# Optimization experiments

Hardware: AMD Instinct MI355X
Metric: run time of the kernel (lower is better)

## Reference

```python
import jax, jax.numpy as jnp
import numpy as np

HEAD_DIM = 128
SCALE = HEAD_DIM ** -0.5  # head_scaling == up_scaling == 1/sqrt(head_dim)


def setup_inputs() -> dict:
    key = jax.random.key(0)
    kq, kk, ku, kv = jax.random.split(key, 4)
    B, H, S, D = 2, 16, 2048, 128
    Hk, I = 4, 2048
    Q = jax.random.normal(kq, (B, H, S, D), dtype=jnp.float32)
    K = jax.random.normal(kk, (Hk, I, D), dtype=jnp.float32)
    U = jax.random.normal(ku, (Hk, I, D), dtype=jnp.float32)
    V = jax.random.normal(kv, (Hk, I, D), dtype=jnp.float32)
    return {"Q": Q, "K": K, "U": U, "V": V}


def reference(Q, K, U, V):
    # Q: (B, H, S, D); K/U/V: (Hk, I, D); GQA grouping G = H // Hk
    B, H, S, D = Q.shape
    Hk, I, _ = K.shape
    G = H // Hk
    Qr = Q.reshape(B, Hk, G, S, D)
    # gate scores and up projection, both scaled by 1/sqrt(D)
    M = jnp.einsum('bkgsd,kid->bkgsi', Qr, K) * SCALE
    N = jnp.einsum('bkgsd,kid->bkgsi', Qr, U) * SCALE
    A = jax.nn.silu(M) * N  # gated activation, (B, Hk, G, S, I)
    out = jnp.einsum('bkgsi,kid->bkgsd', A, V)
    return out.reshape(B, H, S, D)
```

## Files before the change

### kernel.cpp

```cpp
#include <hip/hip_runtime.h>

#define B_   2
#define H_   16
#define G_   4
#define S_   2048
#define D_   128
#define I_   2048

#define BM   128
#define BN   32
#define TPB  256
#define NIT  (I_ / BN)
#define KUT  4096
#define VT   8192
#define HSTR (3 * 262144)

#define KIDX(r,c) ((r)*128 + ((c) ^ (((r)&15)<<3)))
#define VIDX(d,c) ((d)*64  + ((c) ^ (((d)&7)<<3)))

static constexpr float SCALE = 0.08838834764831845f;

typedef __fp16   p2v  __attribute__((ext_vector_type(2)));
typedef _Float16 h8v  __attribute__((ext_vector_type(8)));
typedef float    f4v  __attribute__((ext_vector_type(4)));
typedef float    f16v __attribute__((ext_vector_type(16)));
typedef int      i4v  __attribute__((ext_vector_type(4)));

__device__ __forceinline__ int pkf16(float a, float b) {
    p2v t = __builtin_amdgcn_cvt_pkrtz(a, b);
    int r; __builtin_memcpy(&r, &t, 4); return r;
}

#define GL_LDS(gp, lp) __builtin_amdgcn_global_load_lds(                      \
    (const __attribute__((address_space(1))) void*)(gp),                      \
    (__attribute__((address_space(3))) void*)(lp), 16, 0, 0)

__global__ __launch_bounds__(256) void convert_kernel(
    const float* __restrict__ Kg, const float* __restrict__ Ug,
    const float* __restrict__ Vg, _Float16* __restrict__ ws)
{
    const int bid = blockIdx.x;
    const int tid = threadIdx.x;
    __shared__ float vt[64 * 128];
    if (bid < 256) {
        const int kh = bid >> 6, m = (bid >> 5) & 1, it = bid & 31;
        const float* src = (m ? Ug : Kg) + (size_t)kh * I_ * D_ + (size_t)it * 64 * D_;
        _Float16* dstb = ws + (size_t)kh * HSTR + (size_t)m * 262144 + (size_t)it * 2 * KUT;
        const int r   = tid >> 2;
        const int cb  = (tid & 3) * 32;
        const int swz = (r & 15) << 3;
        _Float16* dst = dstb + (size_t)(r >> 5) * KUT + (r & 31) * 128;
#pragma unroll
        for (int g = 0; g < 4; ++g) {
            const int cc0 = cb + g * 8;
            const int d0  = cc0 ^ swz;
            const float4 a = *(const float4*)(src + r * D_ + d0);
            const float4 c = *(const float4*)(src + r * D_ + d0 + 4);
            h8v v; p2v* v2 = (p2v*)&v;
            v2[0] = __builtin_amdgcn_cvt_pkrtz(a.x, a.y);
            v2[1] = __builtin_amdgcn_cvt_pkrtz(a.z, a.w);
            v2[2] = __builtin_amdgcn_cvt_pkrtz(c.x, c.y);
            v2[3] = __builtin_amdgcn_cvt_pkrtz(c.z, c.w);
            *(h8v*)(dst + cc0) = v;
        }
    } else {
        const int v  = bid - 256;
        const int kh = v >> 5, it = v & 31;
        const float* src = Vg + (size_t)kh * I_ * D_ + (size_t)it * 64 * D_;
#pragma unroll
        for (int p = 0; p < 8; ++p) {
            const int idx = p * 256 + tid;
            const int i   = idx >> 5;
            const int d4  = (idx & 31) * 4;
            *(float4*)(&vt[i * 128 + d4]) = *(const float4*)(src + (size_t)i * D_ + d4);
        }
        __syncthreads();
        _Float16* dst = ws + (size_t)kh * HSTR + 2 * 262144 + (size_t)it * VT;
        const int d   = tid >> 1;
        const int cb  = (tid & 1) * 32;
        const int swz = (d & 7) << 3;
#pragma unroll
        for (int g = 0; g < 4; ++g) {
            const int cc0 = cb + g * 8;
            const int ib  = cc0 ^ swz;
            h8v w; p2v* w2 = (p2v*)&w;
#pragma unroll
            for (int pr = 0; pr < 4; ++pr)
                w2[pr] = __builtin_amdgcn_cvt_pkrtz(vt[(ib + 2 * pr) * 128 + d],
                                                    vt[(ib + 2 * pr + 1) * 128 + d]);
            *(h8v*)(dst + d * 64 + cc0) = w;
        }
    }
}

__global__ __launch_bounds__(TPB, 2) void flashmlp_kernel(
    const float* __restrict__ Qg, const _Float16* __restrict__ ws,
    float* __restrict__ Og)
{
    __shared__ _Float16 Ks[2 * KUT];
    __shared__ _Float16 Us[2 * KUT];
    __shared__ _Float16 Vt[2 * VT];

    const int bid   = blockIdx.x;
    const int xcd   = bid & 7;
    const int kh    = xcd >> 1;
    const int j     = ((bid >> 3) << 1) | (xcd & 1);
    const int stile = j & 15;
    const int bg    = j >> 4;
    const int b     = bg >> 2;
    const int g     = bg & 3;
    const int h     = kh * G_ + g;

    const int tid  = threadIdx.x;
    const int wave = tid >> 6;
    const int lane = tid & 63;
    const int l31  = lane & 31;
    const int hl   = lane >> 5;

    const size_t qbase = ((size_t)(b * H_ + h) * S_ + (size_t)stile * BM) * D_;
    const _Float16* wsK = ws + (size_t)kh * HSTR;
    const _Float16* wsU = wsK + 262144;
    const _Float16* wsV = wsK + 2 * 262144;

    const int soK = wave * 1024 + lane * 8;
    const int suK = wave * 1024;
    const int soV = wave * 2048 + lane * 8;
    const int suV = wave * 2048;

    h8v qf[8];
    {
        const float* qp = Qg + qbase + (size_t)(wave * 32 + l31) * D_;
#pragma unroll
        for (int ks = 0; ks < 8; ++ks) {
            const float4 a = *(const float4*)(qp + ks * 16 + hl * 8);
            const float4 c = *(const float4*)(qp + ks * 16 + hl * 8 + 4);
            h8v v; p2v* v2 = (p2v*)&v;
            v2[0] = __builtin_amdgcn_cvt_pkrtz(a.x * SCALE, a.y * SCALE);
            v2[1] = __builtin_amdgcn_cvt_pkrtz(a.z * SCALE, a.w * SCALE);
            v2[2] = __builtin_amdgcn_cvt_pkrtz(c.x * SCALE, c.y * SCALE);
            v2[3] = __builtin_amdgcn_cvt_pkrtz(c.z * SCALE, c.w * SCALE);
            qf[ks] = v;
        }
    }

    f16v acc_o[4];
#pragma unroll
    for (int dt = 0; dt < 4; ++dt)
#pragma unroll
        for (int e = 0; e < 16; ++e)
            acc_o[dt][e] = 0.f;

    {
        GL_LDS(wsK + soK,       Ks + suK);
        GL_LDS(wsK + soK + 512, Ks + suK + 512);
        GL_LDS(wsU + soK,       Us + suK);
        GL_LDS(wsU + soK + 512, Us + suK + 512);
        GL_LDS(wsV + soV,        Vt + suV);
        GL_LDS(wsV + soV + 512,  Vt + suV + 512);
        GL_LDS(wsV + soV + 1024, Vt + suV + 1024);
        GL_LDS(wsV + soV + 1536, Vt + suV + 1536);
    }
    __syncthreads();

    for (int it = 0; it < NIT; ++it) {
        const _Float16* ksb = Ks + (it & 1) * KUT;
        const _Float16* usb = Us + (it & 1) * KUT;
        const _Float16* vtb = Vt + ((it >> 1) & 1) * VT;

        if (it + 1 < NIT) {
            const int nb = ((it + 1) & 1) * KUT;
            const _Float16* kt = wsK + (size_t)(it + 1) * KUT;
            const _Float16* ut = wsU + (size_t)(it + 1) * KUT;
            GL_LDS(kt + soK,       Ks + nb + suK);
            GL_LDS(kt + soK + 512, Ks + nb + suK + 512);
            GL_LDS(ut + soK,       Us + nb + suK);
            GL_LDS(ut + soK + 512, Us + nb + suK + 512);
        }
        if (!(it & 1) && (it >> 1) + 1 < 32) {
            const int vb = (it >> 1) + 1;
            const _Float16* vt = wsV + (size_t)vb * VT;
            const int nv = (vb & 1) * VT;
            GL_LDS(vt + soV,        Vt + nv + suV);
            GL_LDS(vt + soV + 512,  Vt + nv + suV + 512);
            GL_LDS(vt + soV + 1024, Vt + nv + suV + 1024);
            GL_LDS(vt + soV + 1536, Vt + nv + suV + 1536);
        }

        f16v am, an;
#pragma unroll
        for (int e = 0; e < 16; ++e) { am[e] = 0.f; an[e] = 0.f; }
        __builtin_amdgcn_s_setprio(1);
#pragma unroll
        for (int ks = 0; ks < 8; ++ks) {
            const h8v kf = *(const h8v*)(&ksb[KIDX(l31, ks * 16 + hl * 8)]);
            const h8v uf = *(const h8v*)(&usb[KIDX(l31, ks * 16 + hl * 8)]);
            am = __builtin_amdgcn_mfma_f32_32x32x16_f16(kf, qf[ks], am, 0, 0, 0);
            an = __builtin_amdgcn_mfma_f32_32x32x16_f16(uf, qf[ks], an, 0, 0, 0);
        }
        __builtin_amdgcn_s_setprio(0);

        int P[8];
#pragma unroll
        for (int p = 0; p < 8; ++p) {
            const float m0 = am[2 * p + 0], n0 = an[2 * p + 0];
            const float m1 = am[2 * p + 1], n1 = an[2 * p + 1];
            const float g0 = m0 * __builtin_amdgcn_rcpf(1.f + __expf(-m0)) * n0;
            const float g1 = m1 * __builtin_amdgcn_rcpf(1.f + __expf(-m1)) * n1;
            P[p] = pkf16(g0, g1);
        }
        auto sA = __builtin_amdgcn_permlane32_swap(P[0], P[2], false, false);
        auto sB = __builtin_amdgcn_permlane32_swap(P[1], P[3], false, false);
        auto sC = __builtin_amdgcn_permlane32_swap(P[4], P[6], false, false);
        auto sD = __builtin_amdgcn_permlane32_swap(P[5], P[7], false, false);
        h8v pb0, pb1;
        {
            i4v wlo = i4v{static_cast<int>(sA[0]), static_cast<int>(sB[0]),
                          static_cast<int>(sA[1]), static_cast<int>(sB[1])};
            i4v whi = i4v{static_cast<int>(sC[0]), static_cast<int>(sD[0]),
                          static_cast<int>(sC[1]), static_cast<int>(sD[1])};
            __builtin_memcpy(&pb0, &wlo, 16);
            __builtin_memcpy(&pb1, &whi, 16);
        }

#pragma unroll
        for (int k2 = 0; k2 < 2; ++k2) {
            const int ks2 = (it & 1) * 2 + k2;
            const h8v pb = k2 ? pb1 : pb0;
            h8v va[4];
#pragma unroll
            for (int dt = 0; dt < 4; ++dt)
                va[dt] = *(const h8v*)(&vtb[VIDX(dt * 32 + l31, ks2 * 16 + hl * 8)]);
            __builtin_amdgcn_s_setprio(1);
#pragma unroll
            for (int dt = 0; dt < 4; ++dt)
                acc_o[dt] = __builtin_amdgcn_mfma_f32_32x32x16_f16(va[dt], pb, acc_o[dt], 0, 0, 0);
            __builtin_amdgcn_s_setprio(0);
        }

        __syncthreads();
    }

    {
        const int qrow = stile * BM + wave * 32 + l31;
        float* op = Og + ((size_t)(b * H_ + h) * S_ + qrow) * D_;
#pragma unroll
        for (int dt = 0; dt < 4; ++dt)
#pragma unroll
            for (int g4 = 0; g4 < 4; ++g4) {
                f4v v = f4v{acc_o[dt][4 * g4 + 0], acc_o[dt][4 * g4 + 1],
                            acc_o[dt][4 * g4 + 2], acc_o[dt][4 * g4 + 3]};
                *(f4v*)(op + dt * 32 + g4 * 8 + hl * 4) = v;
            }
    }
}

extern "C" void kernel_launch(void* const* d_in, const int* in_sizes, int n_in,
                              void* d_out, int out_size, void* d_ws, size_t ws_size,
                              hipStream_t stream) {
    const float* Q = (const float*)d_in[0];
    const float* K = (const float*)d_in[1];
    const float* U = (const float*)d_in[2];
    const float* V = (const float*)d_in[3];
    float* out = (float*)d_out;
    _Float16* ws = (_Float16*)d_ws;

    convert_kernel<<<dim3(384), dim3(256), 0, stream>>>(K, U, V, ws);
    flashmlp_kernel<<<dim3((S_ / BM) * B_ * H_), dim3(TPB), 0, stream>>>(Q, ws, out);
}
```

Baseline: 201.6 us.

## Double query tile per wave and split intermediate dimension across two wave groups

Each block now covers 256 query rows with 512 threads. Each wave processes two 32-row query subtiles, so every K/U/V fragment read from LDS is reused twice. The two halves of the block each handle half of the I dimension with their own double-buffered LDS staging, and their partial outputs are reduced through LDS at the end. This cuts LDS and global weight traffic per unit of output but doubles accumulator registers and LDS use to 128KB, which may reduce occupancy to one block per CU.

```diff
diff --git a/kernel.cpp b/kernel.cpp
--- a/kernel.cpp
+++ b/kernel.cpp
@@ -7,10 +7,9 @@
 #define D_   128
 #define I_   2048
 
-#define BM   128
-#define BN   32
-#define TPB  256
-#define NIT  (I_ / BN)
+#define BM   256
+#define TPB  512
+#define NIT  32
 #define KUT  4096
 #define VT   8192
 #define HSTR (3 * 262144)
@@ -97,22 +96,26 @@
     const float* __restrict__ Qg, const _Float16* __restrict__ ws,
     float* __restrict__ Og)
 {
-    __shared__ _Float16 Ks[2 * KUT];
-    __shared__ _Float16 Us[2 * KUT];
-    __shared__ _Float16 Vt[2 * VT];
+    __shared__ __align__(16) char ldsbuf[131072];
+    _Float16* Ks = (_Float16*)ldsbuf;
+    _Float16* Us = (_Float16*)(ldsbuf + 32768);
+    _Float16* Vt = (_Float16*)(ldsbuf + 65536);
+    float*    Rx = (float*)ldsbuf;
 
     const int bid   = blockIdx.x;
     const int xcd   = bid & 7;
     const int kh    = xcd >> 1;
     const int j     = ((bid >> 3) << 1) | (xcd & 1);
-    const int stile = j & 15;
-    const int bg    = j >> 4;
+    const int stile = j & 7;
+    const int bg    = j >> 3;
     const int b     = bg >> 2;
     const int g     = bg & 3;
     const int h     = kh * G_ + g;
 
     const int tid  = threadIdx.x;
     const int wave = tid >> 6;
+    const int wq   = wave & 3;
+    const int wh   = wave >> 2;
     const int lane = tid & 63;
     const int l31  = lane & 31;
     const int hl   = lane >> 5;
@@ -122,14 +125,15 @@
     const _Float16* wsU = wsK + 262144;
     const _Float16* wsV = wsK + 2 * 262144;
 
-    const int soK = wave * 1024 + lane * 8;
-    const int suK = wave * 1024;
-    const int soV = wave * 2048 + lane * 8;
-    const int suV = wave * 2048;
-
-    h8v qf[8];
-    {
-        const float* qp = Qg + qbase + (size_t)(wave * 32 + l31) * D_;
+    const int soK = wq * 1024 + lane * 8;
+    const int suK = wq * 1024;
+    const int soV = wq * 2048 + lane * 8;
+    const int suV = wq * 2048;
+
+    h8v qf[2][8];
+#pragma unroll
+    for (int qs = 0; qs < 2; ++qs) {
+        const float* qp = Qg + qbase + (size_t)(wq * 64 + qs * 32 + l31) * D_;
 #pragma unroll
         for (int ks = 0; ks < 8; ++ks) {
             const float4 a = *(const float4*)(qp + ks * 16 + hl * 8);
@@ -139,118 +143,159 @@
             v2[1] = __builtin_amdgcn_cvt_pkrtz(a.z * SCALE, a.w * SCALE);
             v2[2] = __builtin_amdgcn_cvt_pkrtz(c.x * SCALE, c.y * SCALE);
             v2[3] = __builtin_amdgcn_cvt_pkrtz(c.z * SCALE, c.w * SCALE);
-            qf[ks] = v;
-        }
-    }
-
-    f16v acc_o[4];
-#pragma unroll
-    for (int dt = 0; dt < 4; ++dt)
-#pragma unroll
-        for (int e = 0; e < 16; ++e)
-            acc_o[dt][e] = 0.f;
+            qf[qs][ks] = v;
+        }
+    }
+
+    f16v acc_o[2][4];
+#pragma unroll
+    for (int qs = 0; qs < 2; ++qs)
+#pragma unroll
+        for (int dt = 0; dt < 4; ++dt)
+#pragma unroll
+            for (int e = 0; e < 16; ++e)
+                acc_o[qs][dt][e] = 0.f;
 
     {
-        GL_LDS(wsK + soK,       Ks + suK);
-        GL_LDS(wsK + soK + 512, Ks + suK + 512);
-        GL_LDS(wsU + soK,       Us + suK);
-        GL_LDS(wsU + soK + 512, Us + suK + 512);
-        GL_LDS(wsV + soV,        Vt + suV);
-        GL_LDS(wsV + soV + 512,  Vt + suV + 512);
-        GL_LDS(wsV + soV + 1024, Vt + suV + 1024);
-        GL_LDS(wsV + soV + 1536, Vt + suV + 1536);
+        const _Float16* kt = wsK + (size_t)(wh * 32) * KUT;
+        const _Float16* ut = wsU + (size_t)(wh * 32) * KUT;
+        const _Float16* vt = wsV + (size_t)(wh * 16) * VT;
+        _Float16* kd = Ks + (wh * 2) * 4096;
+        _Float16* ud = Us + (wh * 2) * 4096;
+        _Float16* vd = Vt + (wh * 2) * 8192;
+        GL_LDS(kt + soK,       kd + suK);
+        GL_LDS(kt + soK + 512, kd + suK + 512);
+        GL_LDS(ut + soK,       ud + suK);
+        GL_LDS(ut + soK + 512, ud + suK + 512);
+        GL_LDS(vt + soV,        vd + suV);
+        GL_LDS(vt + soV + 512,  vd + suV + 512);
+        GL_LDS(vt + soV + 1024, vd + suV + 1024);
+        GL_LDS(vt + soV + 1536, vd + suV + 1536);
     }
     __syncthreads();
 
     for (int it = 0; it < NIT; ++it) {
-        const _Float16* ksb = Ks + (it & 1) * KUT;
-        const _Float16* usb = Us + (it & 1) * KUT;
-        const _Float16* vtb = Vt + ((it >> 1) & 1) * VT;
+        const int cur  = it & 1;
+        const int vcur = (it >> 1) & 1;
+        const _Float16* ksb = Ks + (wh * 2 + cur) * 4096;
+        const _Float16* usb = Us + (wh * 2 + cur) * 4096;
+        const _Float16* vtb = Vt + (wh * 2 + vcur) * 8192;
 
         if (it + 1 < NIT) {
-            const int nb = ((it + 1) & 1) * KUT;
-            const _Float16* kt = wsK + (size_t)(it + 1) * KUT;
-            const _Float16* ut = wsU + (size_t)(it + 1) * KUT;
-            GL_LDS(kt + soK,       Ks + nb + suK);
-            GL_LDS(kt + soK + 512, Ks + nb + suK + 512);
-            GL_LDS(ut + soK,       Us + nb + suK);
-            GL_LDS(ut + soK + 512, Us + nb + suK + 512);
-        }
-        if (!(it & 1) && (it >> 1) + 1 < 32) {
+            const int nb = cur ^ 1;
+            const _Float16* kt = wsK + (size_t)(wh * 32 + it + 1) * KUT;
+            const _Float16* ut = wsU + (size_t)(wh * 32 + it + 1) * KUT;
+            _Float16* kd = Ks + (wh * 2 + nb) * 4096;
+            _Float16* ud = Us + (wh * 2 + nb) * 4096;
+            GL_LDS(kt + soK,       kd + suK);
+            GL_LDS(kt + soK + 512, kd + suK + 512);
+            GL_LDS(ut + soK,       ud + suK);
+            GL_LDS(ut + soK + 512, ud + suK + 512);
+        }
+        if (!(it & 1) && (it >> 1) + 1 < 16) {
             const int vb = (it >> 1) + 1;
-            const _Float16* vt = wsV + (size_t)vb * VT;
-            const int nv = (vb & 1) * VT;
-            GL_LDS(vt + soV,        Vt + nv + suV);
-            GL_LDS(vt + soV + 512,  Vt + nv + suV + 512);
-            GL_LDS(vt + soV + 1024, Vt + nv + suV + 1024);
-            GL_LDS(vt + soV + 1536, Vt + nv + suV + 1536);
-        }
-
-        f16v am, an;
-#pragma unroll
-        for (int e = 0; e < 16; ++e) { am[e] = 0.f; an[e] = 0.f; }
+            const _Float16* vt = wsV + (size_t)(wh * 16 + vb) * VT;
+            _Float16* vd = Vt + (wh * 2 + (vb & 1)) * 8192;
+            GL_LDS(vt + soV,        vd + suV);
+            GL_LDS(vt + soV + 512,  vd + suV + 512);
+            GL_LDS(vt + soV + 1024, vd + suV + 1024);
+            GL_LDS(vt + soV + 1536, vd + suV + 1536);
+        }
+
+        f16v am[2], an[2];
+#pragma unroll
+        for (int qs = 0; qs < 2; ++qs)
+#pragma unroll
+            for (int e = 0; e < 16; ++e) { am[qs][e] = 0.f; an[qs][e] = 0.f; }
         __builtin_amdgcn_s_setprio(1);
 #pragma unroll
         for (int ks = 0; ks < 8; ++ks) {
             const h8v kf = *(const h8v*)(&ksb[KIDX(l31, ks * 16 + hl * 8)]);
             const h8v uf = *(const h8v*)(&usb[KIDX(l31, ks * 16 + hl * 8)]);
-            am = __builtin_amdgcn_mfma_f32_32x32x16_f16(kf, qf[ks], am, 0, 0, 0);
-            an = __builtin_amdgcn_mfma_f32_32x32x16_f16(uf, qf[ks], an, 0, 0, 0);
+            am[0] = __builtin_amdgcn_mfma_f32_32x32x16_f16(kf, qf[0][ks], am[0], 0, 0, 0);
+            am[1] = __builtin_amdgcn_mfma_f32_32x32x16_f16(kf, qf[1][ks], am[1], 0, 0, 0);
+            an[0] = __builtin_amdgcn_mfma_f32_32x32x16_f16(uf, qf[0][ks], an[0], 0, 0, 0);
+            an[1] = __builtin_amdgcn_mfma_f32_32x32x16_f16(uf, qf[1][ks], an[1], 0, 0, 0);
         }
         __builtin_amdgcn_s_setprio(0);
 
-        int P[8];
-#pragma unroll
-        for (int p = 0; p < 8; ++p) {
-            const float m0 = am[2 * p + 0], n0 = an[2 * p + 0];
-            const float m1 = am[2 * p + 1], n1 = an[2 * p + 1];
-            const float g0 = m0 * __builtin_amdgcn_rcpf(1.f + __expf(-m0)) * n0;
-            const float g1 = m1 * __builtin_amdgcn_rcpf(1.f + __expf(-m1)) * n1;
-            P[p] = pkf16(g0, g1);
-        }
-        auto sA = __builtin_amdgcn_permlane32_swap(P[0], P[2], false, false);
-        auto sB = __builtin_amdgcn_permlane32_swap(P[1], P[3], false, false);
-        auto sC = __builtin_amdgcn_permlane32_swap(P[4], P[6], false, false);
-        auto sD = __builtin_amdgcn_permlane32_swap(P[5], P[7], false, false);
-        h8v pb0, pb1;
-        {
+        h8v pb[2][2];
+#pragma unroll
+        for (int qs = 0; qs < 2; ++qs) {
+            int P[8];
+#pragma unroll
+            for (int p = 0; p < 8; ++p) {
+                const float m0 = am[qs][2 * p + 0], n0 = an[qs][2 * p + 0];
+                const float m1 = am[qs][2 * p + 1], n1 = an[qs][2 * p + 1];
+                const float g0 = m0 * __builtin_amdgcn_rcpf(1.f + __expf(-m0)) * n0;
+                const float g1 = m1 * __builtin_amdgcn_rcpf(1.f + __expf(-m1)) * n1;
+                P[p] = pkf16(g0, g1);
+            }
+            auto sA = __builtin_amdgcn_permlane32_swap(P[0], P[2], false, false);
+            auto sB = __builtin_amdgcn_permlane32_swap(P[1], P[3], false, false);
+            auto sC = __builtin_amdgcn_permlane32_swap(P[4], P[6], false, false);
+            auto sD = __builtin_amdgcn_permlane32_swap(P[5], P[7], false, false);
             i4v wlo = i4v{static_cast<int>(sA[0]), static_cast<int>(sB[0]),
                           static_cast<int>(sA[1]), static_cast<int>(sB[1])};
             i4v whi = i4v{static_cast<int>(sC[0]), static_cast<int>(sD[0]),
                           static_cast<int>(sC[1]), static_cast<int>(sD[1])};
-            __builtin_memcpy(&pb0, &wlo, 16);
-            __builtin_memcpy(&pb1, &whi, 16);
+            __builtin_memcpy(&pb[qs][0], &wlo, 16);
+            __builtin_memcpy(&pb[qs][1], &whi, 16);
         }
 
 #pragma unroll
         for (int k2 = 0; k2 < 2; ++k2) {
             const int ks2 = (it & 1) * 2 + k2;
-            const h8v pb = k2 ? pb1 : pb0;
             h8v va[4];
 #pragma unroll
             for (int dt = 0; dt < 4; ++dt)
                 va[dt] = *(const h8v*)(&vtb[VIDX(dt * 32 + l31, ks2 * 16 + hl * 8)]);
             __builtin_amdgcn_s_setprio(1);
 #pragma unroll
+            for (int dt = 0; dt < 4; ++dt) {
+                acc_o[0][dt] = __builtin_amdgcn_mfma_f32_32x32x16_f16(va[dt], pb[0][k2], acc_o[0][dt], 0, 0, 0);
+                acc_o[1][dt] = __builtin_amdgcn_mfma_f32_32x32x16_f16(va[dt], pb[1][k2], acc_o[1][dt], 0, 0, 0);
+            }
+            __builtin_amdgcn_s_setprio(0);
+        }
+
+        __syncthreads();
+    }
+
+    if (wh == 1) {
+        const int t = tid & 255;
+#pragma unroll
+        for (int qs = 0; qs < 2; ++qs)
+#pragma unroll
             for (int dt = 0; dt < 4; ++dt)
-                acc_o[dt] = __builtin_amdgcn_mfma_f32_32x32x16_f16(va[dt], pb, acc_o[dt], 0, 0, 0);
-            __builtin_amdgcn_s_setprio(0);
-        }
-
-        __syncthreads();
-    }
-
-    {
-        const int qrow = stile * BM + wave * 32 + l31;
-        float* op = Og + ((size_t)(b * H_ + h) * S_ + qrow) * D_;
-#pragma unroll
-        for (int dt = 0; dt < 4; ++dt)
-#pragma unroll
-            for (int g4 = 0; g4 < 4; ++g4) {
-                f4v v = f4v{acc_o[dt][4 * g4 + 0], acc_o[dt][4 * g4 + 1],
-                            acc_o[dt][4 * g4 + 2], acc_o[dt][4 * g4 + 3]};
-                *(f4v*)(op + dt * 32 + g4 * 8 + hl * 4) = v;
-            }
+#pragma unroll
+                for (int g4 = 0; g4 < 4; ++g4) {
+                    const int c = (qs * 4 + dt) * 4 + g4;
+                    f4v v = f4v{acc_o[qs][dt][4 * g4 + 0], acc_o[qs][dt][4 * g4 + 1],
+                                acc_o[qs][dt][4 * g4 + 2], acc_o[qs][dt][4 * g4 + 3]};
+                    *(f4v*)(&Rx[c * 1024 + t * 4]) = v;
+                }
+    }
+    __syncthreads();
+    if (wh == 0) {
+        const int t = tid;
+#pragma unroll
+        for (int qs = 0; qs < 2; ++qs) {
+            const int qrow = stile * BM + wq * 64 + qs * 32 + l31;
+            float* op = Og + ((size_t)(b * H_ + h) * S_ + qrow) * D_;
+#pragma unroll
+            for (int dt = 0; dt < 4; ++dt)
+#pragma unroll
+                for (int g4 = 0; g4 < 4; ++g4) {
+                    const int c = (qs * 4 + dt) * 4 + g4;
+                    const f4v r = *(const f4v*)(&Rx[c * 1024 + t * 4]);
+                    f4v v = f4v{acc_o[qs][dt][4 * g4 + 0] + r[0],
+                                acc_o[qs][dt][4 * g4 + 1] + r[1],
+                                acc_o[qs][dt][4 * g4 + 2] + r[2],
+                                acc_o[qs][dt][4 * g4 + 3] + r[3]};
+                    *(f4v*)(op + dt * 32 + g4 * 8 + hl * 4) = v;
+                }
+        }
     }
 }
 
```

After: 228.0 us. +13.1%, slower.

## Software-pipeline gate/PV of previous tile with QK/QU MFMAs of current tile

Applied to the files above, without the earlier changes.

Restructures the main loop so each iteration issues the Q·K and Q·U MFMAs for tile t, then runs the SiLU gating and P·V MFMAs for tile t-1 from registers. The V fragments for the next step are preloaded into registers, and two register sets ping-pong through a manually unrolled pair of iterations, with a prologue and an epilogue. The goal is to overlap the VALU transcendental work and permlane shuffles with independent MFMA work, hiding the dependency stall between gate scores and the PV product. The cost is substantially higher VGPR pressure (duplicate accumulators and 16 V fragments) under a 2-blocks-per-CU launch bound, which risks spills or lost occupancy.

```diff
diff --git a/kernel.cpp b/kernel.cpp
--- a/kernel.cpp
+++ b/kernel.cpp
@@ -93,6 +93,82 @@
     }
 }
 
+#define GATE_PV(amP, anP, vaP)                                                \
+{                                                                             \
+    int P[8];                                                                 \
+    _Pragma("unroll")                                                         \
+    for (int p = 0; p < 8; ++p) {                                             \
+        const float m0 = amP[2*p+0], n0 = anP[2*p+0];                         \
+        const float m1 = amP[2*p+1], n1 = anP[2*p+1];                         \
+        const float g0 = m0 * __builtin_amdgcn_rcpf(1.f + __expf(-m0)) * n0;  \
+        const float g1 = m1 * __builtin_amdgcn_rcpf(1.f + __expf(-m1)) * n1;  \
+        P[p] = pkf16(g0, g1);                                                 \
+    }                                                                         \
+    auto sA_ = __builtin_amdgcn_permlane32_swap(P[0], P[2], false, false);    \
+    auto sB_ = __builtin_amdgcn_permlane32_swap(P[1], P[3], false, false);    \
+    auto sC_ = __builtin_amdgcn_permlane32_swap(P[4], P[6], false, false);    \
+    auto sD_ = __builtin_amdgcn_permlane32_swap(P[5], P[7], false, false);    \
+    h8v pb0, pb1;                                                             \
+    {                                                                         \
+        i4v wlo = i4v{(int)sA_[0], (int)sB_[0], (int)sA_[1], (int)sB_[1]};    \
+        i4v whi = i4v{(int)sC_[0], (int)sD_[0], (int)sC_[1], (int)sD_[1]};    \
+        __builtin_memcpy(&pb0, &wlo, 16);                                     \
+        __builtin_memcpy(&pb1, &whi, 16);                                     \
+    }                                                                         \
+    __builtin_amdgcn_s_setprio(1);                                            \
+    _Pragma("unroll")                                                         \
+    for (int dt = 0; dt < 4; ++dt) {                                          \
+        acc_o[dt] = __builtin_amdgcn_mfma_f32_32x32x16_f16(vaP[dt],   pb0, acc_o[dt], 0, 0, 0); \
+        acc_o[dt] = __builtin_amdgcn_mfma_f32_32x32x16_f16(vaP[4+dt], pb1, acc_o[dt], 0, 0, 0); \
+    }                                                                         \
+    __builtin_amdgcn_s_setprio(0);                                            \
+}
+
+#define FITER(T, amP, anP, vaP, amC, anC, vaC)                                \
+{                                                                             \
+    const int t_ = (T);                                                       \
+    const _Float16* ksb = Ks + (t_ & 1) * KUT;                                \
+    const _Float16* usb = Us + (t_ & 1) * KUT;                                \
+    const _Float16* vtb = Vt + ((t_ >> 1) & 1) * VT;                          \
+    if (t_ + 1 < NIT) {                                                       \
+        const int nb = (t_ + 1) & 1;                                          \
+        const _Float16* kt = wsK + (size_t)(t_ + 1) * KUT;                    \
+        const _Float16* ut = wsU + (size_t)(t_ + 1) * KUT;                    \
+        GL_LDS(kt + soK,       Ks + nb * KUT + suK);                          \
+        GL_LDS(kt + soK + 512, Ks + nb * KUT + suK + 512);                    \
+        GL_LDS(ut + soK,       Us + nb * KUT + suK);                          \
+        GL_LDS(ut + soK + 512, Us + nb * KUT + suK + 512);                    \
+    }                                                                         \
+    if (((t_) & 1) == 0 && (t_ >> 1) + 1 < 32) {                              \
+        const int vb = (t_ >> 1) + 1;                                         \
+        const _Float16* vtp = wsV + (size_t)vb * VT;                          \
+        _Float16* vd = Vt + (vb & 1) * VT;                                    \
+        GL_LDS(vtp + soV,        vd + suV);                                   \
+        GL_LDS(vtp + soV + 512,  vd + suV + 512);                             \
+        GL_LDS(vtp + soV + 1024, vd + suV + 1024);                            \
+        GL_LDS(vtp + soV + 1536, vd + suV + 1536);                            \
+    }                                                                         \
+    _Pragma("unroll")                                                         \
+    for (int e = 0; e < 16; ++e) { amC[e] = 0.f; anC[e] = 0.f; }              \
+    __builtin_amdgcn_s_setprio(1);                                            \
+    _Pragma("unroll")                                                         \
+    for (int ks = 0; ks < 8; ++ks) {                                          \
+        const h8v kf = *(const h8v*)(&ksb[KIDX(l31, ks * 16 + hl * 8)]);      \
+        const h8v uf = *(const h8v*)(&usb[KIDX(l31, ks * 16 + hl * 8)]);      \
+        amC = __builtin_amdgcn_mfma_f32_32x32x16_f16(kf, qf[ks], amC, 0, 0, 0); \
+        anC = __builtin_amdgcn_mfma_f32_32x32x16_f16(uf, qf[ks], anC, 0, 0, 0); \
+    }                                                                         \
+    __builtin_amdgcn_s_setprio(0);                                            \
+    GATE_PV(amP, anP, vaP);                                                   \
+    _Pragma("unroll")                                                         \
+    for (int k2 = 0; k2 < 2; ++k2)                                            \
+        _Pragma("unroll")                                                     \
+        for (int dt = 0; dt < 4; ++dt)                                        \
+            vaC[k2 * 4 + dt] = *(const h8v*)(&vtb[VIDX(dt * 32 + l31,         \
+                ((t_ & 1) * 2 + k2) * 16 + hl * 8)]);                         \
+    __syncthreads();                                                          \
+}
+
 __global__ __launch_bounds__(TPB, 2) void flashmlp_kernel(
     const float* __restrict__ Qg, const _Float16* __restrict__ ws,
     float* __restrict__ Og)
@@ -150,6 +226,9 @@
         for (int e = 0; e < 16; ++e)
             acc_o[dt][e] = 0.f;
 
+    f16v amA, anA, amB, anB;
+    h8v  vaA[8], vaB[8];
+
     {
         GL_LDS(wsK + soK,       Ks + suK);
         GL_LDS(wsK + soK + 512, Ks + suK + 512);
@@ -162,83 +241,46 @@
     }
     __syncthreads();
 
-    for (int it = 0; it < NIT; ++it) {
-        const _Float16* ksb = Ks + (it & 1) * KUT;
-        const _Float16* usb = Us + (it & 1) * KUT;
-        const _Float16* vtb = Vt + ((it >> 1) & 1) * VT;
-
-        if (it + 1 < NIT) {
-            const int nb = ((it + 1) & 1) * KUT;
-            const _Float16* kt = wsK + (size_t)(it + 1) * KUT;
-            const _Float16* ut = wsU + (size_t)(it + 1) * KUT;
-            GL_LDS(kt + soK,       Ks + nb + suK);
-            GL_LDS(kt + soK + 512, Ks + nb + suK + 512);
-            GL_LDS(ut + soK,       Us + nb + suK);
-            GL_LDS(ut + soK + 512, Us + nb + suK + 512);
-        }
-        if (!(it & 1) && (it >> 1) + 1 < 32) {
-            const int vb = (it >> 1) + 1;
-            const _Float16* vt = wsV + (size_t)vb * VT;
-            const int nv = (vb & 1) * VT;
-            GL_LDS(vt + soV,        Vt + nv + suV);
-            GL_LDS(vt + soV + 512,  Vt + nv + suV + 512);
-            GL_LDS(vt + soV + 1024, Vt + nv + suV + 1024);
-            GL_LDS(vt + soV + 1536, Vt + nv + suV + 1536);
-        }
-
-        f16v am, an;
-#pragma unroll
-        for (int e = 0; e < 16; ++e) { am[e] = 0.f; an[e] = 0.f; }
+    {
+        const _Float16* kt = wsK + KUT;
+        const _Float16* ut = wsU + KUT;
+        GL_LDS(kt + soK,       Ks + KUT + suK);
+        GL_LDS(kt + soK + 512, Ks + KUT + suK + 512);
+        GL_LDS(ut + soK,       Us + KUT + suK);
+        GL_LDS(ut + soK + 512, Us + KUT + suK + 512);
+        const _Float16* vtp = wsV + VT;
+        GL_LDS(vtp + soV,        Vt + VT + suV);
+        GL_LDS(vtp + soV + 512,  Vt + VT + suV + 512);
+        GL_LDS(vtp + soV + 1024, Vt + VT + suV + 1024);
+        GL_LDS(vtp + soV + 1536, Vt + VT + suV + 1536);
+
+#pragma unroll
+        for (int e = 0; e < 16; ++e) { amA[e] = 0.f; anA[e] = 0.f; }
         __builtin_amdgcn_s_setprio(1);
 #pragma unroll
         for (int ks = 0; ks < 8; ++ks) {
-            const h8v kf = *(const h8v*)(&ksb[KIDX(l31, ks * 16 + hl * 8)]);
-            const h8v uf = *(const h8v*)(&usb[KIDX(l31, ks * 16 + hl * 8)]);
-            am = __builtin_amdgcn_mfma_f32_32x32x16_f16(kf, qf[ks], am, 0, 0, 0);
-            an = __builtin_amdgcn_mfma_f32_32x32x16_f16(uf, qf[ks], an, 0, 0, 0);
+            const h8v kf = *(const h8v*)(&Ks[KIDX(l31, ks * 16 + hl * 8)]);
+            const h8v uf = *(const h8v*)(&Us[KIDX(l31, ks * 16 + hl * 8)]);
+            amA = __builtin_amdgcn_mfma_f32_32x32x16_f16(kf, qf[ks], amA, 0, 0, 0);
+            anA = __builtin_amdgcn_mfma_f32_32x32x16_f16(uf, qf[ks], anA, 0, 0, 0);
         }
         __builtin_amdgcn_s_setprio(0);
-
-        int P[8];
-#pragma unroll
-        for (int p = 0; p < 8; ++p) {
-            const float m0 = am[2 * p + 0], n0 = an[2 * p + 0];
-            const float m1 = am[2 * p + 1], n1 = an[2 * p + 1];
-            const float g0 = m0 * __builtin_amdgcn_rcpf(1.f + __expf(-m0)) * n0;
-            const float g1 = m1 * __builtin_amdgcn_rcpf(1.f + __expf(-m1)) * n1;
-            P[p] = pkf16(g0, g1);
-        }
-        auto sA = __builtin_amdgcn_permlane32_swap(P[0], P[2], false, false);
-        auto sB = __builtin_amdgcn_permlane32_swap(P[1], P[3], false, false);
-        auto sC = __builtin_amdgcn_permlane32_swap(P[4], P[6], false, false);
-        auto sD = __builtin_amdgcn_permlane32_swap(P[5], P[7], false, false);
-        h8v pb0, pb1;
-        {
-            i4v wlo = i4v{static_cast<int>(sA[0]), static_cast<int>(sB[0]),
-                          static_cast<int>(sA[1]), static_cast<int>(sB[1])};
-            i4v whi = i4v{static_cast<int>(sC[0]), static_cast<int>(sD[0]),
-                          static_cast<int>(sC[1]), static_cast<int>(sD[1])};
-            __builtin_memcpy(&pb0, &wlo, 16);
-            __builtin_memcpy(&pb1, &whi, 16);
-        }
-
-#pragma unroll
-        for (int k2 = 0; k2 < 2; ++k2) {
-            const int ks2 = (it & 1) * 2 + k2;
-            const h8v pb = k2 ? pb1 : pb0;
-            h8v va[4];
+#pragma unroll
+        for (int k2 = 0; k2 < 2; ++k2)
 #pragma unroll
             for (int dt = 0; dt < 4; ++dt)
-                va[dt] = *(const h8v*)(&vtb[VIDX(dt * 32 + l31, ks2 * 16 + hl * 8)]);
-            __builtin_amdgcn_s_setprio(1);
-#pragma unroll
-            for (int dt = 0; dt < 4; ++dt)
-                acc_o[dt] = __builtin_amdgcn_mfma_f32_32x32x16_f16(va[dt], pb, acc_o[dt], 0, 0, 0);
-            __builtin_amdgcn_s_setprio(0);
-        }
-
+                vaA[k2 * 4 + dt] = *(const h8v*)(&Vt[VIDX(dt * 32 + l31,
+                    k2 * 16 + hl * 8)]);
         __syncthreads();
     }
+
+    for (int t = 1; t + 1 < NIT; t += 2) {
+        FITER(t,     amA, anA, vaA, amB, anB, vaB);
+        FITER(t + 1, amB, anB, vaB, amA, anA, vaA);
+    }
+    FITER(NIT - 1, amA, anA, vaA, amB, anB, vaB);
+
+    GATE_PV(amB, anB, vaB);
 
     {
         const int qrow = stile * BM + wave * 32 + l31;
```

Measured after the change: 221.6 us. +9.9%, slower.
